# Performance work log

Hardware: AMD Instinct MI355X
Metric: run time of the kernel (lower is better)

The kernel has to match this reference:

```python
import jax, jax.numpy as jnp
import numpy as np

B, S, H, E = 64, 1024, 256, 256

def setup_inputs() -> dict:
    key = jax.random.key(0)
    k = jax.random.split(key, 6)
    scale = 1.0 / np.sqrt(H)
    return {
        "data_alpha": jax.random.normal(k[0], (B, S, H), jnp.float32),
        "data_beta": jax.random.normal(k[1], (B, S, H), jnp.float32),
        "data_embed": jax.random.normal(k[2], (B, S, E), jnp.float32),
        "data_mask": jnp.ones((B, S), jnp.float32),
        "Wb": jax.random.normal(k[3], (E, H), jnp.float32) * scale,
        "bb": jnp.zeros((E,), jnp.float32),
        "Wa": jax.random.normal(k[4], (H,), jnp.float32) * scale,
        "ba": jnp.zeros((1,), jnp.float32),
    }

def reference(data_alpha, data_beta, data_embed, data_mask, Wb, bb, Wa, ba):
    # beta gates: tanh(Linear(H->E))  [B,S,E]
    beta_w = jnp.tanh(jnp.einsum('bsh,eh->bse', data_beta, Wb) + bb)
    # alpha logits: Linear(H->1)  [B,S]
    corr = jnp.einsum('bsh,h->bs', data_alpha, Wa) + ba
    attn = jnp.exp(corr)[:, None, :]                       # [B,1,S]
    seq = data_alpha.shape[1]
    flag = jnp.triu(jnp.ones((seq, seq), data_alpha.dtype))[None]  # j >= i
    ef = flag * data_mask[:, None, :]                      # [B,S,S]
    num = attn * ef                                        # [B,S,S]
    acc = jnp.sum(num, axis=-1, keepdims=True) + 1e-10     # [B,S,1]
    alpha = num / acc                                      # [B,S,S]
    ew = beta_w * data_embed                               # [B,S,E]
    return jnp.einsum('bij,bje->bie', alpha, ew)           # [B,S,E]
```

## Files before the change

kernel.cpp:

```cpp
#include <hip/hip_runtime.h>
#include <hip/hip_bf16.h>

#define S_LEN 1024
#define B_DIM 64
#define H_DIM 256
#define E_DIM 256
#define M_ROWS (B_DIM * S_LEN)

#define CT_COLS 64
#define NCT (E_DIM / CT_COLS)
#define CHUNK_R 256
#define NCHUNKS (S_LEN / CHUNK_R)
#define NTHREADS 1024
#define NWAVES 16

#define BPAD 264

typedef __attribute__((ext_vector_type(8))) short bf16x8;
typedef __attribute__((ext_vector_type(4))) float f32x4;

__device__ __forceinline__ short cvt1(float f) {
  union { float ff; unsigned u; } t;
  t.ff = f;
  unsigned u = t.u;
  return (short)((u + 0x7fffu + ((u >> 16) & 1u)) >> 16);
}

__device__ __forceinline__ bf16x8 cvt8v(float4 x, float4 y) {
  bf16x8 r;
  r[0] = cvt1(x.x); r[1] = cvt1(x.y); r[2] = cvt1(x.z); r[3] = cvt1(x.w);
  r[4] = cvt1(y.x); r[5] = cvt1(y.y); r[6] = cvt1(y.z); r[7] = cvt1(y.w);
  return r;
}

__device__ __forceinline__ float fast_tanh(float x) {
  float t = __expf(2.0f * x);
  return 1.0f - 2.0f * __builtin_amdgcn_rcpf(t + 1.0f);
}

__global__ __launch_bounds__(256) void w_kernel(
    const float* __restrict__ alpha, const float* __restrict__ Wa,
    const float* __restrict__ ba, const float* __restrict__ mask,
    float* __restrict__ wv) {
  int wave = threadIdx.x >> 6, lane = threadIdx.x & 63;
  long long row = (long long)blockIdx.x * 4 + wave;
  const float4 a = reinterpret_cast<const float4*>(alpha + row * H_DIM)[lane];
  const float4 wa = reinterpret_cast<const float4*>(Wa)[lane];
  float d = a.x * wa.x + a.y * wa.y + a.z * wa.z + a.w * wa.w;
#pragma unroll
  for (int m = 32; m; m >>= 1) d += __shfl_xor(d, m);
  if (lane == 0) wv[row] = expf(d + ba[0]) * mask[row];
}

__global__ __launch_bounds__(1024) void acc_kernel(
    const float* __restrict__ wv, float* __restrict__ invacc) {
  __shared__ float s[2][S_LEN];
  int b = blockIdx.x, i = threadIdx.x;
  s[0][i] = wv[b * S_LEN + i];
  __syncthreads();
  int src = 0;
#pragma unroll
  for (int off = 1; off < S_LEN; off <<= 1) {
    float v = s[src][i];
    if (i + off < S_LEN) v += s[src][i + off];
    s[src ^ 1][i] = v;
    __syncthreads();
    src ^= 1;
  }
  invacc[b * S_LEN + i] = 1.0f / (s[src][i] + 1e-10f);
}

__global__ __launch_bounds__(NTHREADS, 4) void fused_kernel(
    const float* __restrict__ beta, const float* __restrict__ Wb,
    const float* __restrict__ bb, const float* __restrict__ embed,
    const float* __restrict__ wv, const float* __restrict__ invacc,
    float* __restrict__ out) {
  __shared__ short Bsm[CT_COLS * BPAD];
  __shared__ float segsum[2][NWAVES * CT_COLS];
  __shared__ float carry[2][CT_COLS];

  const int tid = threadIdx.x;
  const int hw = blockIdx.x;
  const int b = (hw & 7) + (((hw >> 3) & 7) << 3);
  const int colbase = (hw >> 6) * CT_COLS;

  {
    int c = tid >> 4, ks = (tid & 15) * 16;
    const float4* src =
        reinterpret_cast<const float4*>(Wb + (long long)(colbase + c) * H_DIM + ks);
    float4 v0 = src[0], v1 = src[1], v2 = src[2], v3 = src[3];
    *reinterpret_cast<bf16x8*>(&Bsm[c * BPAD + ks]) = cvt8v(v0, v1);
    *reinterpret_cast<bf16x8*>(&Bsm[c * BPAD + ks + 8]) = cvt8v(v2, v3);
  }
  if (tid < CT_COLS) { carry[0][tid] = 0.f; carry[1][tid] = 0.f; }
  __syncthreads();

  const int wave = tid >> 6, lane = tid & 63;
  const int rl = lane & 15, kg = lane >> 4;

  float bbv[4];
#pragma unroll
  for (int j = 0; j < 4; ++j) bbv[j] = bb[colbase + j * 16 + rl];

  const float* ap =
      beta + ((long long)b * S_LEN + 3 * CHUNK_R + wave * 16 + rl) * H_DIM + kg * 8;
  float4 pa0 = *reinterpret_cast<const float4*>(ap + 0);
  float4 pa1 = *reinterpret_cast<const float4*>(ap + 4);
  float4 pb0 = *reinterpret_cast<const float4*>(ap + 32);
  float4 pb1 = *reinterpret_cast<const float4*>(ap + 36);

  float emb[4][4], wvq[4], inv[4];
  {
    const long long r0 = (long long)b * S_LEN + 3 * CHUNK_R + wave * 16 + kg * 4;
#pragma unroll
    for (int q = 0; q < 4; ++q) {
      wvq[q] = wv[r0 + q];
      inv[q] = invacc[r0 + q];
#pragma unroll
      for (int j = 0; j < 4; ++j)
        emb[q][j] = embed[(r0 + q) * E_DIM + colbase + j * 16 + rl];
    }
  }

  for (int chunk = NCHUNKS - 1; chunk >= 0; --chunk) {
    const int nc = (chunk > 0) ? chunk - 1 : 0;
    const long long rowstart = (long long)b * S_LEN + chunk * CHUNK_R;
    const long long r0 = rowstart + wave * 16;
    const float* ap_next =
        beta + ((long long)b * S_LEN + nc * CHUNK_R + wave * 16 + rl) * H_DIM + kg * 8;

    f32x4 acc[4] = {{0.f,0.f,0.f,0.f},{0.f,0.f,0.f,0.f},
                    {0.f,0.f,0.f,0.f},{0.f,0.f,0.f,0.f}};

#pragma unroll
    for (int ks = 0; ks < 8; ++ks) {
      float4 n0, n1;
      if (ks < 6) {
        n0 = *reinterpret_cast<const float4*>(ap + (ks + 2) * 32);
        n1 = *reinterpret_cast<const float4*>(ap + (ks + 2) * 32 + 4);
      } else {
        n0 = *reinterpret_cast<const float4*>(ap_next + (ks - 6) * 32);
        n1 = *reinterpret_cast<const float4*>(ap_next + (ks - 6) * 32 + 4);
      }
      bf16x8 am = cvt8v(pa0, pa1);
      int kb = ks * 32 + kg * 8;
#pragma unroll
      for (int j = 0; j < 4; ++j) {
        bf16x8 bn = *reinterpret_cast<const bf16x8*>(&Bsm[(j * 16 + rl) * BPAD + kb]);
        acc[j] = __builtin_amdgcn_mfma_f32_16x16x32_bf16(am, bn, acc[j], 0, 0, 0);
      }
      pa0 = pb0; pa1 = pb1; pb0 = n0; pb1 = n1;
    }
    ap = ap_next;

    float emb_n[4][4], wvq_n[4], inv_n[4];
    {
      const long long rn = (long long)b * S_LEN + nc * CHUNK_R + wave * 16 + kg * 4;
#pragma unroll
      for (int q = 0; q < 4; ++q) {
        wvq_n[q] = wv[rn + q];
        inv_n[q] = invacc[rn + q];
#pragma unroll
        for (int j = 0; j < 4; ++j)
          emb_n[q][j] = embed[(rn + q) * E_DIM + colbase + j * 16 + rl];
      }
    }

    const int rd = chunk & 1;
    float sv[4][4], off[4];
#pragma unroll
    for (int j = 0; j < 4; ++j) {
      int c = j * 16 + rl;
      float p[4];
#pragma unroll
      for (int q = 0; q < 4; ++q)
        p[q] = wvq[q] * fast_tanh(acc[j][q] + bbv[j]) * emb[q][j];
      sv[j][3] = p[3];
      sv[j][2] = p[2] + sv[j][3];
      sv[j][1] = p[1] + sv[j][2];
      sv[j][0] = p[0] + sv[j][1];
      float gtot = sv[j][0];
      float t16 = __shfl_xor(gtot, 16);
      float t32 = __shfl_xor(gtot, 32);
      float t48 = __shfl_xor(gtot, 48);
      off[j] = (kg == 0) ? (t16 + t32 + t48)
             : (kg == 1) ? (t32 + t48)
             : (kg == 2) ? t16 : 0.f;
      float wtot = gtot + t16 + t32 + t48;
      if (kg == 0) segsum[rd][wave * CT_COLS + c] = wtot;
    }
    __syncthreads();

#pragma unroll
    for (int j = 0; j < 4; ++j) {
      int c = j * 16 + rl;
      float segoff = carry[rd][c];
#pragma unroll
      for (int w2 = 0; w2 < NWAVES; ++w2) {
        float t = segsum[rd][w2 * CT_COLS + c];
        segoff += (w2 > wave) ? t : 0.f;
      }
      off[j] += segoff;
      if (wave == 0 && kg == 0) carry[rd ^ 1][c] = off[j] + sv[j][0];
#pragma unroll
      for (int q = 0; q < 4; ++q) {
        long long r = r0 + kg * 4 + q;
        out[r * E_DIM + colbase + c] = (sv[j][q] + off[j]) * inv[q];
      }
    }

#pragma unroll
    for (int q = 0; q < 4; ++q) {
      wvq[q] = wvq_n[q]; inv[q] = inv_n[q];
#pragma unroll
      for (int j = 0; j < 4; ++j) emb[q][j] = emb_n[q][j];
    }
  }
}

extern "C" void kernel_launch(void* const* d_in, const int* in_sizes, int n_in,
                              void* d_out, int out_size, void* d_ws,
                              size_t ws_size, hipStream_t stream) {
  const float* alpha = (const float*)d_in[0];
  const float* beta = (const float*)d_in[1];
  const float* embed = (const float*)d_in[2];
  const float* mask = (const float*)d_in[3];
  const float* Wb = (const float*)d_in[4];
  const float* bb = (const float*)d_in[5];
  const float* Wa = (const float*)d_in[6];
  const float* ba = (const float*)d_in[7];
  float* out = (float*)d_out;

  float* wv = (float*)d_ws;
  float* invacc = wv + M_ROWS;

  w_kernel<<<M_ROWS / 4, 256, 0, stream>>>(alpha, Wa, ba, mask, wv);
  acc_kernel<<<B_DIM, 1024, 0, stream>>>(wv, invacc);
  fused_kernel<<<B_DIM * NCT, NTHREADS, 0, stream>>>(beta, Wb, bb, embed, wv,
                                                     invacc, out);
}
```

Before: 242.9 us.

## Halve column tile to 32, swizzle Wb LDS layout, drop embed prefetch

```diff
diff --git a/kernel.cpp b/kernel.cpp
--- a/kernel.cpp
+++ b/kernel.cpp
@@ -7,14 +7,12 @@
 #define E_DIM 256
 #define M_ROWS (B_DIM * S_LEN)
 
-#define CT_COLS 64
+#define CT_COLS 32
 #define NCT (E_DIM / CT_COLS)
 #define CHUNK_R 256
 #define NCHUNKS (S_LEN / CHUNK_R)
 #define NTHREADS 1024
 #define NWAVES 16
-
-#define BPAD 264
 
 typedef __attribute__((ext_vector_type(8))) short bf16x8;
 typedef __attribute__((ext_vector_type(4))) float f32x4;
@@ -70,37 +68,39 @@
   invacc[b * S_LEN + i] = 1.0f / (s[src][i] + 1e-10f);
 }
 
-__global__ __launch_bounds__(NTHREADS, 4) void fused_kernel(
+__global__ __launch_bounds__(NTHREADS, 8) void fused_kernel(
     const float* __restrict__ beta, const float* __restrict__ Wb,
     const float* __restrict__ bb, const float* __restrict__ embed,
     const float* __restrict__ wv, const float* __restrict__ invacc,
     float* __restrict__ out) {
-  __shared__ short Bsm[CT_COLS * BPAD];
+  __shared__ short Bsm[CT_COLS * H_DIM];
   __shared__ float segsum[2][NWAVES * CT_COLS];
   __shared__ float carry[2][CT_COLS];
 
   const int tid = threadIdx.x;
   const int hw = blockIdx.x;
-  const int b = (hw & 7) + (((hw >> 3) & 7) << 3);
+  const int b = ((hw & 7) << 3) | ((hw >> 3) & 7);
   const int colbase = (hw >> 6) * CT_COLS;
 
   {
-    int c = tid >> 4, ks = (tid & 15) * 16;
+    int row = tid >> 5;
+    int g = tid & 31;
     const float4* src =
-        reinterpret_cast<const float4*>(Wb + (long long)(colbase + c) * H_DIM + ks);
-    float4 v0 = src[0], v1 = src[1], v2 = src[2], v3 = src[3];
-    *reinterpret_cast<bf16x8*>(&Bsm[c * BPAD + ks]) = cvt8v(v0, v1);
-    *reinterpret_cast<bf16x8*>(&Bsm[c * BPAD + ks + 8]) = cvt8v(v2, v3);
+        reinterpret_cast<const float4*>(Wb + (long long)(colbase + row) * H_DIM + g * 8);
+    float4 v0 = src[0], v1 = src[1];
+    int gs = g ^ (row & 7);
+    *reinterpret_cast<bf16x8*>(&Bsm[row * H_DIM + gs * 8]) = cvt8v(v0, v1);
   }
   if (tid < CT_COLS) { carry[0][tid] = 0.f; carry[1][tid] = 0.f; }
   __syncthreads();
 
   const int wave = tid >> 6, lane = tid & 63;
   const int rl = lane & 15, kg = lane >> 4;
-
-  float bbv[4];
-#pragma unroll
-  for (int j = 0; j < 4; ++j) bbv[j] = bb[colbase + j * 16 + rl];
+  const int sw = rl & 7;
+
+  float bbv[2];
+#pragma unroll
+  for (int j = 0; j < 2; ++j) bbv[j] = bb[colbase + j * 16 + rl];
 
   const float* ap =
       beta + ((long long)b * S_LEN + 3 * CHUNK_R + wave * 16 + rl) * H_DIM + kg * 8;
@@ -109,28 +109,13 @@
   float4 pb0 = *reinterpret_cast<const float4*>(ap + 32);
   float4 pb1 = *reinterpret_cast<const float4*>(ap + 36);
 
-  float emb[4][4], wvq[4], inv[4];
-  {
-    const long long r0 = (long long)b * S_LEN + 3 * CHUNK_R + wave * 16 + kg * 4;
-#pragma unroll
-    for (int q = 0; q < 4; ++q) {
-      wvq[q] = wv[r0 + q];
-      inv[q] = invacc[r0 + q];
-#pragma unroll
-      for (int j = 0; j < 4; ++j)
-        emb[q][j] = embed[(r0 + q) * E_DIM + colbase + j * 16 + rl];
-    }
-  }
-
   for (int chunk = NCHUNKS - 1; chunk >= 0; --chunk) {
     const int nc = (chunk > 0) ? chunk - 1 : 0;
-    const long long rowstart = (long long)b * S_LEN + chunk * CHUNK_R;
-    const long long r0 = rowstart + wave * 16;
+    const long long r0 = (long long)b * S_LEN + chunk * CHUNK_R + wave * 16;
     const float* ap_next =
         beta + ((long long)b * S_LEN + nc * CHUNK_R + wave * 16 + rl) * H_DIM + kg * 8;
 
-    f32x4 acc[4] = {{0.f,0.f,0.f,0.f},{0.f,0.f,0.f,0.f},
-                    {0.f,0.f,0.f,0.f},{0.f,0.f,0.f,0.f}};
+    f32x4 acc[2] = {{0.f,0.f,0.f,0.f},{0.f,0.f,0.f,0.f}};
 
 #pragma unroll
     for (int ks = 0; ks < 8; ++ks) {
@@ -143,38 +128,35 @@
         n1 = *reinterpret_cast<const float4*>(ap_next + (ks - 6) * 32 + 4);
       }
       bf16x8 am = cvt8v(pa0, pa1);
-      int kb = ks * 32 + kg * 8;
-#pragma unroll
-      for (int j = 0; j < 4; ++j) {
-        bf16x8 bn = *reinterpret_cast<const bf16x8*>(&Bsm[(j * 16 + rl) * BPAD + kb]);
+      int g0 = (ks * 4 + kg);
+#pragma unroll
+      for (int j = 0; j < 2; ++j) {
+        bf16x8 bn = *reinterpret_cast<const bf16x8*>(
+            &Bsm[(j * 16 + rl) * H_DIM + (g0 ^ sw) * 8]);
         acc[j] = __builtin_amdgcn_mfma_f32_16x16x32_bf16(am, bn, acc[j], 0, 0, 0);
       }
       pa0 = pb0; pa1 = pb1; pb0 = n0; pb1 = n1;
     }
     ap = ap_next;
 
-    float emb_n[4][4], wvq_n[4], inv_n[4];
-    {
-      const long long rn = (long long)b * S_LEN + nc * CHUNK_R + wave * 16 + kg * 4;
-#pragma unroll
-      for (int q = 0; q < 4; ++q) {
-        wvq_n[q] = wv[rn + q];
-        inv_n[q] = invacc[rn + q];
-#pragma unroll
-        for (int j = 0; j < 4; ++j)
-          emb_n[q][j] = embed[(rn + q) * E_DIM + colbase + j * 16 + rl];
-      }
-    }
-
     const int rd = chunk & 1;
-    float sv[4][4], off[4];
-#pragma unroll
-    for (int j = 0; j < 4; ++j) {
+    const long long rq = r0 + kg * 4;
+    float wvq[4], inv[4];
+#pragma unroll
+    for (int q = 0; q < 4; ++q) {
+      wvq[q] = wv[rq + q];
+      inv[q] = invacc[rq + q];
+    }
+
+    float sv[2][4], off[2];
+#pragma unroll
+    for (int j = 0; j < 2; ++j) {
       int c = j * 16 + rl;
+      int e = colbase + c;
       float p[4];
 #pragma unroll
       for (int q = 0; q < 4; ++q)
-        p[q] = wvq[q] * fast_tanh(acc[j][q] + bbv[j]) * emb[q][j];
+        p[q] = wvq[q] * fast_tanh(acc[j][q] + bbv[j]) * embed[(rq + q) * E_DIM + e];
       sv[j][3] = p[3];
       sv[j][2] = p[2] + sv[j][3];
       sv[j][1] = p[1] + sv[j][2];
@@ -192,7 +174,7 @@
     __syncthreads();
 
 #pragma unroll
-    for (int j = 0; j < 4; ++j) {
+    for (int j = 0; j < 2; ++j) {
       int c = j * 16 + rl;
       float segoff = carry[rd][c];
 #pragma unroll
@@ -203,17 +185,8 @@
       off[j] += segoff;
       if (wave == 0 && kg == 0) carry[rd ^ 1][c] = off[j] + sv[j][0];
 #pragma unroll
-      for (int q = 0; q < 4; ++q) {
-        long long r = r0 + kg * 4 + q;
-        out[r * E_DIM + colbase + c] = (sv[j][q] + off[j]) * inv[q];
-      }
-    }
-
-#pragma unroll
-    for (int q = 0; q < 4; ++q) {
-      wvq[q] = wvq_n[q]; inv[q] = inv_n[q];
-#pragma unroll
-      for (int j = 0; j < 4; ++j) emb[q][j] = emb_n[q][j];
+      for (int q = 0; q < 4; ++q)
+        out[(rq + q) * E_DIM + colbase + c] = (sv[j][q] + off[j]) * inv[q];
     }
   }
 }
```

Result: slower. 296.5 us (+22.0%).
